# Performance work log

Measured on AMD Instinct MI355X. Metric: run time of the kernel, lower is better.

The kernel has to match this reference:

```python
import jax, jax.numpy as jnp
import numpy as np

D_MODEL = 512; D_STATE = 32; D_HEAD = 64; G = 4; R = 2
D_INNER = 2 * D_MODEL            # expand=2 -> 1024
H = D_INNER // D_HEAD            # 16 heads
RATIO = H // G                   # 4 heads per group
CHUNK = 128; EPS = 1e-5
DIM_Z = D_INNER; DIM_X = D_INNER
DIM_B = G * D_STATE * R; DIM_C = DIM_B
D_PROJ = DIM_Z + DIM_X + DIM_B + DIM_C + G + G
BATCH = 1; SEQ = 2048


def setup_inputs() -> dict:
    key = jax.random.key(0)
    ks = jax.random.split(key, 10)
    u = jax.random.normal(ks[0], (BATCH, SEQ, D_MODEL), jnp.float32)
    W_in = jax.random.normal(ks[1], (D_MODEL, D_PROJ), jnp.float32) * 0.02
    b_in = jnp.zeros((D_PROJ,), jnp.float32)
    # dt bias init: inverse-softplus of log-uniform dt in [1e-3, 1e-1]
    dt0 = jnp.exp(jax.random.uniform(ks[2], (G,)) * (np.log(0.1) - np.log(0.001)) + np.log(0.001))
    inv_dt = dt0 + jnp.log(-jnp.expm1(-dt0))
    s = DIM_Z + DIM_X + DIM_B + DIM_C
    b_in = b_in.at[s:s + G].set(inv_dt).at[s + G:].set(-3.0)
    W_xup = jax.random.normal(ks[3], (D_HEAD, D_HEAD * R), jnp.float32) * (1.0 / np.sqrt(D_HEAD * R))
    W_ydown = jax.random.normal(ks[4], (D_HEAD * R, D_HEAD), jnp.float32) * (1.0 / np.sqrt(D_HEAD * R))
    A_log = jnp.log(jax.random.uniform(ks[5], (G,), minval=1.0, maxval=16.0))
    theta_log = jax.random.normal(ks[6], (G, D_STATE // 2), jnp.float32)
    D_param = jnp.ones((H,), jnp.float32)
    wB = jnp.ones((D_STATE * R,), jnp.float32)
    wC = jnp.ones((D_STATE * R,), jnp.float32)
    bias_B = jnp.ones((G, D_STATE, R), jnp.float32)
    bias_C = jnp.ones((G, D_STATE, R), jnp.float32)
    W_out = jax.random.normal(ks[7], (D_INNER, D_MODEL), jnp.float32) * 0.02
    return dict(u=u, W_in=W_in, b_in=b_in, W_xup=W_xup, W_ydown=W_ydown,
                A_log=A_log, theta_log=theta_log, D_param=D_param,
                wB=wB, wC=wC, bias_B=bias_B, bias_C=bias_C, W_out=W_out)


def rmsnorm(x, w):
    return x * jax.lax.rsqrt(jnp.mean(x * x, -1, keepdims=True) + EPS) * w


def apply_rope(x, angles):
    # x: (B,L,G,N,R)  angles: (B,L,G,N/2)  -- rotate (even, odd) pairs along N
    Bz, L, Gg, N, Rr = x.shape
    xr = x.reshape(Bz, L, Gg, N // 2, 2, Rr)
    re, im = xr[..., 0, :], xr[..., 1, :]
    c = jnp.cos(angles)[..., None]
    s = jnp.sin(angles)[..., None]
    out = jnp.stack([re * c - im * s, re * s + im * c], axis=-2)
    return out.reshape(Bz, L, Gg, N, Rr)


def segsum(x):
    # x: (..., T) log-decay -> (..., T, T) causal pairwise cumulative sums
    T = x.shape[-1]
    cs = jnp.cumsum(x, -1)
    seg = cs[..., :, None] - cs[..., None, :]
    mask = jnp.tril(jnp.ones((T, T), bool))
    return jnp.where(mask, seg, -jnp.inf)


def chunk_parallel_scan(u_in, dt, A, C):
    # u_in: (B,L,H,N,P)  dt: (B,L,H)  A: (H,)  C: (B,L,H,N,R)
    Bz, L, Hh, N, P = u_in.shape
    Rr = C.shape[-1]
    nc = L // CHUNK
    la = (dt * A).reshape(Bz, nc, CHUNK, Hh)                       # log alpha per chunk
    uc = u_in.reshape(Bz, nc, CHUNK, Hh, N, P)
    Cc = C.reshape(Bz, nc, CHUNK, Hh, N, Rr)
    Lm = jnp.exp(segsum(la.transpose(0, 1, 3, 2)))                 # (B,nc,H,cs,cs)
    h_intra = jnp.einsum('bchts,bcshnp->bcthnp', Lm, uc)           # intra-chunk states
    y_diag = jnp.einsum('bcthnp,bcthnr->bcthpr', h_intra, Cc)
    decay_chunk = jnp.exp(la.sum(2))                               # (B,nc,H)
    h_final = h_intra[:, :, -1]                                    # (B,nc,H,N,P)
    h0 = jnp.zeros((Bz, Hh, N, P), u_in.dtype)

    def step(h, inp):
        d, c = inp
        return h * d[..., None, None] + c, h

    h_last, h_states = jax.lax.scan(
        step, h0, (decay_chunk.transpose(1, 0, 2), h_final.transpose(1, 0, 2, 3, 4)))
    h_states = h_states.transpose(1, 0, 2, 3, 4)                   # state entering each chunk
    decay_intra = jnp.exp(jnp.cumsum(la, 2))                       # (B,nc,cs,H)
    C_scaled = Cc * decay_intra[..., None, None]
    y_off = jnp.einsum('bchnp,bcthnr->bcthpr', h_states, C_scaled)
    y = (y_diag + y_off).reshape(Bz, L, Hh, P, Rr)
    return y, h_last


def _forward(u, W_in, b_in, W_xup, W_ydown, A_log, theta_log, D_param, wB, wC, bias_B, bias_C, W_out):
    Bz, L, _ = u.shape
    N, P = D_STATE, D_HEAD
    proj = u @ W_in + b_in
    o = 0
    z = proj[..., o:o + DIM_Z]; o += DIM_Z
    x = proj[..., o:o + DIM_X]; o += DIM_X
    Bi = proj[..., o:o + DIM_B]; o += DIM_B
    Ci = proj[..., o:o + DIM_C]; o += DIM_C
    dt_raw = proj[..., o:o + G]; o += G
    lam_raw = proj[..., o:o + G]

    dt = jax.nn.softplus(dt_raw)                                   # (B,L,G)
    lam = jax.nn.sigmoid(lam_raw)                                  # trapezoidal coeff
    x = jax.nn.silu(x)

    Bm = rmsnorm(Bi.reshape(Bz, L, G, N * R), wB).reshape(Bz, L, G, N, R) + bias_B
    Cm = rmsnorm(Ci.reshape(Bz, L, G, N * R), wC).reshape(Bz, L, G, N, R) + bias_C

    # data-dependent RoPE: cumulative angles = cumsum_t(dt_t * theta)
    theta = jnp.exp(theta_log)                                     # (G, N/2)
    angles = jnp.cumsum(dt[..., None] * theta, axis=1)             # (B,L,G,N/2)
    Br = apply_rope(Bm, angles)
    Cr = apply_rope(Cm, angles)

    # expand group-shared dynamics to heads
    Bh = jnp.repeat(Br, RATIO, axis=2)                             # (B,L,H,N,R)
    Ch = jnp.repeat(Cr, RATIO, axis=2)
    dth = jnp.repeat(dt, RATIO, axis=2)                            # (B,L,H)
    lamh = jnp.repeat(lam, RATIO, axis=2)
    Ah = jnp.repeat(-jnp.exp(A_log), RATIO)                        # (H,)

    xh = x.reshape(Bz, L, H, P)
    x_up = (xh @ W_xup).reshape(Bz, L, H, P, R)                    # MIMO up-projection
    u_ssm = jnp.einsum('blhnr,blhpr->blhnp', Bh, x_up) * dth[..., None, None]
    # generalized trapezoidal rule: blend current and previous input contribution
    u_prev = jnp.pad(u_ssm[:, :-1], ((0, 0), (1, 0), (0, 0), (0, 0), (0, 0)))
    w = lamh[..., None, None]
    u_trap = w * u_ssm + (1.0 - w) * u_prev

    y, _h = chunk_parallel_scan(u_trap, dth, Ah, Ch)               # (B,L,H,P,R)
    y = y.reshape(Bz, L, H, P * R) @ W_ydown                       # MIMO down-projection
    y = y + D_param[None, None, :, None] * xh                      # skip connection
    y = y * jax.nn.silu(z.reshape(Bz, L, H, P))                    # gate
    return (y.reshape(Bz, L, D_INNER)) @ W_out


def reference(u, W_in, b_in, W_xup, W_ydown, A_log, theta_log, D_param, wB, wC, bias_B, bias_C, W_out):
    return _forward(u, W_in, b_in, W_xup, W_ydown, A_log, theta_log,
                    D_param, wB, wC, bias_B, bias_C, W_out)
```

## Files before the change

### kernel.cpp

```cpp
#include <hip/hip_runtime.h>
#include <hip/hip_bf16.h>

typedef __hip_bfloat16 bf16;
typedef __bf16 bfv8 __attribute__((ext_vector_type(8)));
typedef float fv4 __attribute__((ext_vector_type(4)));

__device__ __forceinline__ float bf2f(bf16 x){ return __bfloat162float(x); }
__device__ __forceinline__ bf16 f2bf(float x){ return __float2bfloat16(x); }
__device__ __forceinline__ float blo(unsigned u){ return __uint_as_float(u<<16); }
__device__ __forceinline__ float bhi(unsigned u){ return __uint_as_float(u & 0xffff0000u); }
struct __align__(8) bf4v { bf16 x,y,z,w; };
struct __align__(16) bf8s { ushort u[8]; };
__device__ __forceinline__ float4 ldb4(const bf16* p){
  ushort4 u = *(const ushort4*)p;
  float4 r;
  r.x = __uint_as_float(((unsigned)u.x)<<16);
  r.y = __uint_as_float(((unsigned)u.y)<<16);
  r.z = __uint_as_float(((unsigned)u.z)<<16);
  r.w = __uint_as_float(((unsigned)u.w)<<16);
  return r;
}
__device__ __forceinline__ void stb4(bf16* p, float4 v){
  bf4v t; t.x=f2bf(v.x); t.y=f2bf(v.y); t.z=f2bf(v.z); t.w=f2bf(v.w);
  *(bf4v*)p = t;
}

#define L_SEQ 2048
#define DPROJ 2568
#define NCHUNK 16
#define TCH 128

__device__ __forceinline__ void tbody(const float* __restrict__ in, bf16* __restrict__ out,
                                      int R, int C, int Cpad, int bx, int by, float (*t)[33])
{
  int c0 = bx*32, r0 = by*32;
  int tx = threadIdx.x & 31, ty = threadIdx.x >> 5;
  for (int i=0;i<32;i+=8){
    int r = r0+i+ty, cc = c0+tx;
    t[i+ty][tx] = (r<R && cc<C) ? in[(size_t)r*C+cc] : 0.f;
  }
  __syncthreads();
  for (int i=0;i<32;i+=8){
    int cc = c0+i+ty, r = r0+tx;
    if (cc<Cpad && r<R) out[(size_t)cc*R + r] = f2bf(t[tx][i+ty]);
  }
}

__global__ void prep(const float* __restrict__ u, bf16* __restrict__ ubf,
                     const float* __restrict__ Win, bf16* __restrict__ WinT,
                     const float* __restrict__ Wout, bf16* __restrict__ WoutT,
                     const float* __restrict__ Wyd, bf16* __restrict__ WydT)
{
  __shared__ float t[32][33];
  int b = blockIdx.x;
  if (b < 1024){
    int i = (b*256 + threadIdx.x)*4;
    float4 v = *(const float4*)&u[i];
    stb4(&ubf[i], v);
  } else if (b < 2368){
    int idx = b - 1024;
    tbody(Win, WinT, 512, DPROJ, 2688, idx%84, idx/84, t);
  } else if (b < 2880){
    int idx = b - 2368;
    tbody(Wout, WoutT, 1024, 512, 512, idx%16, idx/16, t);
  } else {
    int idx = b - 2880;
    tbody(Wyd, WydT, 128, 64, 64, idx%2, idx/2, t);
  }
}

__global__ void __launch_bounds__(256) gemm1_mfma(const bf16* __restrict__ A, const bf16* __restrict__ BT,
                                                  const float* __restrict__ bias, bf16* __restrict__ C,
                                                  float* __restrict__ side)
{
  const int K = 512;
  __shared__ __align__(16) bf16 As[128*40];
  __shared__ __align__(16) bf16 Bs[128*40];
  int tid = threadIdx.x;
  int col0 = blockIdx.x*128, row0 = blockIdx.y*128;
  int wid = tid>>6, lane = tid&63;
  int wm = (wid&1)*64, wn = (wid>>1)*64;
  int lm = lane&15, lq = lane>>4;
  fv4 acc[4][4] = {};
  for (int k0=0;k0<K;k0+=32){
    #pragma unroll
    for (int i=0;i<2;i++){
      int e = tid + i*256;
      int r = e>>2, k8 = (e&3)*8;
      *(bf8s*)&As[r*40+k8] = *(const bf8s*)&A[(size_t)(row0+r)*K + k0 + k8];
      *(bf8s*)&Bs[r*40+k8] = *(const bf8s*)&BT[(size_t)(col0+r)*K + k0 + k8];
    }
    __syncthreads();
    bfv8 af[4], bfr[4];
    #pragma unroll
    for (int mf=0;mf<4;mf++) af[mf] = *(const bfv8*)&As[(wm+mf*16+lm)*40 + lq*8];
    #pragma unroll
    for (int nf=0;nf<4;nf++) bfr[nf] = *(const bfv8*)&Bs[(wn+nf*16+lm)*40 + lq*8];
    #pragma unroll
    for (int mf=0;mf<4;mf++)
      #pragma unroll
      for (int nf=0;nf<4;nf++)
        acc[mf][nf] = __builtin_amdgcn_mfma_f32_16x16x32_bf16(af[mf], bfr[nf], acc[mf][nf], 0,0,0);
    __syncthreads();
  }
  #pragma unroll
  for (int mf=0;mf<4;mf++){
    #pragma unroll
    for (int nf=0;nf<4;nf++){
      int gcol = col0 + wn + nf*16 + lm;
      if (gcol < DPROJ){
        float bia = bias[gcol];
        #pragma unroll
        for (int r=0;r<4;r++){
          int grow = row0 + wm + mf*16 + lq*4 + r;
          float v = acc[mf][nf][r] + bia;
          C[(size_t)grow*DPROJ + gcol] = f2bf(v);
          if (gcol >= 2560) side[grow*8 + (gcol-2560)] = v;
        }
      }
    }
  }
}

__global__ void __launch_bounds__(256) gemmo_mfma(const bf16* __restrict__ Yp, const bf16* __restrict__ BT,
                                                  float* __restrict__ C)
{
  const int K = 1024;
  __shared__ __align__(16) bf16 As[64*40];
  __shared__ __align__(16) bf16 Bs[64*40];
  int tid = threadIdx.x;
  int col0 = blockIdx.x*64, row0 = blockIdx.y*64;
  int wid = tid>>6, lane = tid&63;
  int wm = (wid&1)*32, wn = (wid>>1)*32;
  int lm = lane&15, lq = lane>>4;
  fv4 acc[2][2] = {};
  for (int k0=0;k0<K;k0+=32){
    {
      int m = tid>>2, k8 = (tid&3)*8;
      int kg = k0 + k8;
      *(bf8s*)&As[m*40+k8] = *(const bf8s*)&Yp[(size_t)(row0+m)*2048 + ((kg>>6)*128) + 64 + (kg&63)];
    }
    {
      int n = tid>>2, k8 = (tid&3)*8;
      *(bf8s*)&Bs[n*40+k8] = *(const bf8s*)&BT[(size_t)(col0+n)*K + k0 + k8];
    }
    __syncthreads();
    bfv8 af[2], bfr[2];
    #pragma unroll
    for (int mf=0;mf<2;mf++) af[mf] = *(const bfv8*)&As[(wm+mf*16+lm)*40 + lq*8];
    #pragma unroll
    for (int nf=0;nf<2;nf++) bfr[nf] = *(const bfv8*)&Bs[(wn+nf*16+lm)*40 + lq*8];
    #pragma unroll
    for (int mf=0;mf<2;mf++)
      #pragma unroll
      for (int nf=0;nf<2;nf++)
        acc[mf][nf] = __builtin_amdgcn_mfma_f32_16x16x32_bf16(af[mf], bfr[nf], acc[mf][nf], 0,0,0);
    __syncthreads();
  }
  #pragma unroll
  for (int mf=0;mf<2;mf++)
    #pragma unroll
    for (int nf=0;nf<2;nf++){
      int gcol = col0 + wn + nf*16 + lm;
      #pragma unroll
      for (int r=0;r<4;r++){
        int grow = row0 + wm + mf*16 + lq*4 + r;
        C[(size_t)grow*512 + gcol] = acc[mf][nf][r];
      }
    }
}

__global__ void k23(const float* __restrict__ dlraw, float* __restrict__ dtb,
                    float* __restrict__ lamb, float* __restrict__ csdt)
{
  __shared__ float raw[L_SEQ*8];
  __shared__ float dts[L_SEQ*4];
  __shared__ float segs[4][64];
  int tid = threadIdx.x;
  for (int e=tid;e<L_SEQ*8;e+=256) raw[e] = dlraw[e];
  __syncthreads();
  int g = tid & 3, seg = tid >> 2;
  for (int i = 0; i < 32; i++){
    int l = seg*32 + i;
    float dr = raw[l*8 + g];
    float lr = raw[l*8 + 4 + g];
    float dt = (dr > 15.f) ? dr : log1pf(__expf(dr));
    dts[l*4+g] = dt;
    dtb[l*4+g] = dt;
    lamb[l*4+g] = 1.f/(1.f+__expf(-lr));
  }
  __syncthreads();
  float s = 0.f;
  for (int i=0;i<32;i++) s += dts[(seg*32+i)*4 + g];
  segs[g][seg] = s;
  __syncthreads();
  if (tid < 4) { float run = 0.f; for (int q=0;q<64;q++){ float t = segs[tid][q]; segs[tid][q] = run; run += t; } }
  __syncthreads();
  float run = segs[g][seg];
  for (int i=0;i<32;i++){ int l = seg*32+i; run += dts[l*4+g]; csdt[l*4+g] = run; }
}

__global__ void __launch_bounds__(256) k45(
  const bf16* __restrict__ proj, const float* __restrict__ wB, const float* __restrict__ wC,
  const float* __restrict__ biasB, const float* __restrict__ biasC,
  const float* __restrict__ theta_log, const float* __restrict__ csdt,
  const float* __restrict__ Wx,
  bf16* __restrict__ Br, bf16* __restrict__ Cr, bf16* __restrict__ xup)
{
  __shared__ __align__(16) float wsm[64*128];
  __shared__ float xs[1024];
  int l = blockIdx.x, tid = threadIdx.x;
  const bf16* pr = proj + (size_t)l*DPROJ;
  for (int e=tid;e<8192;e+=256) wsm[e] = Wx[e];
  for (int e=tid;e<1024;e+=256){ float v = bf2f(pr[1024+e]); xs[e] = v/(1.f+__expf(-v)); }
  {
    int g = tid >> 6, idx = tid & 63;
    float bv = bf2f(pr[2048 + g*64 + idx]);
    float cv = bf2f(pr[2304 + g*64 + idx]);
    float sb = bv*bv, sc = cv*cv;
    #pragma unroll
    for (int off=32; off; off>>=1){ sb += __shfl_xor(sb, off); sc += __shfl_xor(sc, off); }
    float rb = rsqrtf(sb*(1.f/64.f) + 1e-5f);
    float rc = rsqrtf(sc*(1.f/64.f) + 1e-5f);
    float bm = bv*rb*wB[idx] + biasB[g*64+idx];
    float cm = cv*rc*wC[idx] + biasC[g*64+idx];
    int k = idx >> 2;
    float ang = csdt[l*4+g] * __expf(theta_log[g*16+k]);
    float ca = cosf(ang), sa = sinf(ang);
    float bp = __shfl_xor(bm, 2);
    float cp = __shfl_xor(cm, 2);
    bool is_im = (idx >> 1) & 1;
    float bo = is_im ? (bp*sa + bm*ca) : (bm*ca - bp*sa);
    float co = is_im ? (cp*sa + cm*ca) : (cm*ca - cp*sa);
    Br[((size_t)l*4+g)*64 + idx] = f2bf(bo);
    Cr[((size_t)l*4+g)*64 + idx] = f2bf(co);
  }
  __syncthreads();
  {
    int h = tid>>4, prb = (tid&15)*8;
    float acc[8] = {};
    for (int k=0;k<64;k++){
      float xv = xs[h*64+k];
      const float4* w4 = (const float4*)&wsm[k*128 + prb];
      float4 a = w4[0], b = w4[1];
      acc[0]+=xv*a.x; acc[1]+=xv*a.y; acc[2]+=xv*a.z; acc[3]+=xv*a.w;
      acc[4]+=xv*b.x; acc[5]+=xv*b.y; acc[6]+=xv*b.z; acc[7]+=xv*b.w;
    }
    bf16* o = xup + ((size_t)l*16+h)*128 + prb;
    stb4(o,   make_float4(acc[0],acc[1],acc[2],acc[3]));
    stb4(o+4, make_float4(acc[4],acc[5],acc[6],acc[7]));
  }
}

__global__ void __launch_bounds__(256) k6y(
  const bf16* __restrict__ Br, const bf16* __restrict__ Cr, const bf16* __restrict__ xup,
  const float* __restrict__ dtb, const float* __restrict__ lamb, const float* __restrict__ A_log,
  bf16* __restrict__ ypr, bf16* __restrict__ hfin, float* __restrict__ dcb, float* __restrict__ csb)
{
  __shared__ __align__(16) bf16 Cs[64*40];
  __shared__ __align__(16) bf16 Bs[64*40];
  __shared__ __align__(16) bf16 Bsn[32*72];
  __shared__ __align__(16) bf16 Fs[64*72];
  __shared__ __align__(16) bf16 Xs[64*72];
  __shared__ float dt_l[128], lam_l[128], cs_l[128];
  __shared__ float u1s[160], u12s[160], vs_[32];
  int bx = blockIdx.x; int g = bx & 3, q = bx >> 2;
  int c = blockIdx.y;
  int h4 = blockIdx.z;
  int h = g*4 + h4;
  int tid = threadIdx.x;
  int l0 = c*TCH;
  int w = tid>>6, lane = tid&63, lm = lane&15, lq = lane>>4;
  float Ah = -__expf(A_log[g]);
  float dt_prev = (c>0) ? dtb[(l0-1)*4+g] : 0.f;
  if (tid<128){ dt_l[tid] = dtb[(l0+tid)*4+g]; lam_l[tid] = lamb[(l0+tid)*4+g]; }
  __syncthreads();
  if (tid<128) cs_l[tid] = dt_l[tid]*Ah;
  __syncthreads();
  for (int off=1; off<128; off<<=1){
    float add = 0.f;
    if (tid<128 && tid>=off) add = cs_l[tid-off];
    __syncthreads();
    if (tid<128) cs_l[tid] += add;
    __syncthreads();
  }
  float ref = cs_l[q*32+16];
  if (tid < 160){
    int jj = tid;
    float u1v = 0.f, u2v = 0.f;
    if (jj>=1 && jj<=128) u1v = lam_l[jj-1]*dt_l[jj-1]*__expf(fminf(ref-cs_l[jj-1],60.f));
    if (jj<=127){ float dtx = (jj>=1)? dt_l[jj-1] : dt_prev; u2v = (1.f-lam_l[jj])*dtx*__expf(fminf(ref-cs_l[jj],60.f)); }
    u1s[jj] = u1v; u12s[jj] = u1v+u2v;
  }
  if (tid < 32) vs_[tid] = __expf(fminf(cs_l[q*32+tid]-ref,60.f));
  for (int e4 = tid; e4 < 512; e4 += 256){
    int tl = e4>>4, c4 = (e4&15)*4;
    bf4v v = *(const bf4v*)&Cr[((size_t)(l0+q*32+tl)*4+g)*64 + c4];
    bf16 arr[4] = {v.x,v.y,v.z,v.w};
    #pragma unroll
    for (int i=0;i<4;i++){ int q6=c4+i; Cs[((tl<<1)|(q6&1))*40 + (q6>>1)] = arr[i]; }
  }
  __syncthreads();
  float vfin = __expf(fminf(cs_l[127]-ref,60.f));
  fv4 acc[4] = {};
  fv4 acch[2] = {};
  int nch = (q+2 < 5) ? (q+2) : 5;
  for (int kc=0; kc<nch; kc++){
    for (int e4 = tid; e4 < 512; e4 += 256){
      int jjloc = e4>>4, c4 = (e4&15)*4;
      int jj = kc*32 + jjloc; int l = l0-1+jj;
      bf4v v;
      if (l >= 0 && jj <= 128) v = *(const bf4v*)&Br[((size_t)l*4+g)*64 + c4];
      else { v.x=v.y=v.z=v.w = f2bf(0.f); }
      bf16 arr[4] = {v.x,v.y,v.z,v.w};
      #pragma unroll
      for (int i=0;i<4;i++){ int q6=c4+i; Bs[((q6&1)*32+jjloc)*40 + (q6>>1)] = arr[i]; }
      if (q == 3){
        float gcv = vfin * u12s[jj];
        #pragma unroll
        for (int i=0;i<4;i++){ int q6=c4+i; Bsn[(q6>>1)*72 + (q6&1)*32 + jjloc] = f2bf(gcv*bf2f(arr[i])); }
      }
    }
    for (int e4 = tid; e4 < 1024; e4 += 256){
      int jjloc = e4>>5, c4 = (e4&31)*4;
      int jj = kc*32+jjloc; int l = l0-1+jj;
      bf4v v;
      if (l>=0 && jj<=128) v = *(const bf4v*)&xup[((size_t)l*16 + h)*128 + c4];
      else { v.x=v.y=v.z=v.w = f2bf(0.f); }
      bf16 arr[4] = {v.x,v.y,v.z,v.w};
      #pragma unroll
      for (int i=0;i<4;i++){ int q7=c4+i; Xs[(q7>>1)*72 + (q7&1)*32 + jjloc] = arr[i]; }
    }
    __syncthreads();
    {
      bfv8 a = *(const bfv8*)&Cs[(w*16+lm)*40 + lq*8];
      fv4 zz = {0.f,0.f,0.f,0.f};
      int rb = w*16 + lq*4;
      float vA = vs_[rb>>1];
      float vB = vs_[(rb>>1)+1];
      #pragma unroll
      for (int nt=0;nt<4;nt++){
        bfv8 b = *(const bfv8*)&Bs[(nt*16+lm)*40 + lq*8];
        fv4 s = __builtin_amdgcn_mfma_f32_16x16x32_bf16(a, b, zz, 0,0,0);
        int col = nt*16+lm;
        int jj = kc*32 + (col&31);
        float u1v = u1s[jj], u12v = u12s[jj];
        #pragma unroll
        for (int r=0;r<4;r++){
          int row = rb + r;
          float vT = (r<2) ? vA : vB;
          float cf;
          if (kc < q) cf = u12v;
          else {
            int T = q*32 + (row>>1);
            if (kc == q) cf = (jj<=T) ? u12v : ((jj==T+1) ? u1v : 0.f);
            else         cf = (jj==T+1) ? u1v : 0.f;
          }
          Fs[row*72+col] = f2bf(cf*vT*s[r]);
        }
      }
    }
    __syncthreads();
    #pragma unroll
    for (int r2=0;r2<2;r2++){
      bfv8 a = *(const bfv8*)&Fs[(w*16+lm)*72 + r2*32 + lq*8];
      #pragma unroll
      for (int nt=0;nt<4;nt++){
        bfv8 b = *(const bfv8*)&Xs[(nt*16+lm)*72 + r2*32 + lq*8];
        acc[nt] = __builtin_amdgcn_mfma_f32_16x16x32_bf16(a, b, acc[nt], 0,0,0);
      }
    }
    if (q == 3){
      #pragma unroll
      for (int r2=0;r2<2;r2++){
        bfv8 a = *(const bfv8*)&Xs[(w*16+lm)*72 + r2*32 + lq*8];
        #pragma unroll
        for (int nt2=0;nt2<2;nt2++){
          bfv8 b = *(const bfv8*)&Bsn[(nt2*16+lm)*72 + r2*32 + lq*8];
          acch[nt2] = __builtin_amdgcn_mfma_f32_16x16x32_bf16(a, b, acch[nt2], 0,0,0);
        }
      }
    }
    __syncthreads();
  }
  #pragma unroll
  for (int nt=0;nt<4;nt++){
    int p = nt*16+lm;
    #pragma unroll
    for (int r=0;r<4;r++){
      int row = w*16+lq*4+r;
      int T = q*32+(row>>1), r1 = row&1;
      ypr[((size_t)(l0+T)*16 + h)*128 + p*2+r1] = f2bf(acc[nt][r]);
    }
  }
  if (q == 3){
    #pragma unroll
    for (int nt2=0;nt2<2;nt2++){
      int n = nt2*16+lm;
      #pragma unroll
      for (int r=0;r<4;r++){
        int p = w*16+lq*4+r;
        hfin[(((size_t)c*16+h)*64 + p)*32 + n] = f2bf(acch[nt2][r]);
      }
    }
    if (tid == 0) dcb[c*16+h] = __expf(cs_l[127]);
  }
  if (q == 0 && h4 == 0 && tid < 128) csb[(c*4+g)*128 + tid] = cs_l[tid];
}

__global__ void __launch_bounds__(256) k8af(
  const bf16* __restrict__ Cr, const bf16* __restrict__ hfin,
  const float* __restrict__ dcb, const float* __restrict__ csb,
  bf16* __restrict__ ypr, const bf16* __restrict__ WydT,
  const bf16* __restrict__ proj, const float* __restrict__ Dp)
{
  __shared__ __align__(16) char arena[52224];
  bf16* C2s = (bf16*)arena;
  bf16* hT  = (bf16*)(arena + 20480);
  float* cse = (float*)(arena + 25600);
  bf16* Yf  = (bf16*)arena;
  bf16* Wds = (bf16*)(arena + 34816);
  int h = blockIdx.x, c = blockIdx.y;
  int g = h >> 2;
  int tid = threadIdx.x;
  int l0 = c*TCH;
  int w = tid>>6, lane = tid&63, lm = lane&15, lq = lane>>4;
  for (int e4 = tid; e4 < 2048; e4 += 256){
    int tl = e4>>4, c4 = (e4&15)*4;
    bf4v v = *(const bf4v*)&Cr[((size_t)(l0+tl)*4+g)*64 + c4];
    bf16 arr[4] = {v.x,v.y,v.z,v.w};
    #pragma unroll
    for (int i=0;i<4;i++){ int q6=c4+i; C2s[((tl<<1)|(q6&1))*40 + (q6>>1)] = arr[i]; }
  }
  for (int e = tid; e < 1024; e += 256){
    int qq = e>>4, k8 = (e&15)*8;
    *(bf8s*)&Wds[qq*136 + k8] = *(const bf8s*)&WydT[qq*128 + k8];
  }
  {
    int e0 = tid*8;
    float carry[8] = {};
    for (int j = 0; j < c; j++){
      float dc = dcb[j*16+h];
      float4 a = ldb4(&hfin[((size_t)j*16+h)*2048 + e0]);
      float4 b = ldb4(&hfin[((size_t)j*16+h)*2048 + e0 + 4]);
      carry[0]=carry[0]*dc+a.x; carry[1]=carry[1]*dc+a.y; carry[2]=carry[2]*dc+a.z; carry[3]=carry[3]*dc+a.w;
      carry[4]=carry[4]*dc+b.x; carry[5]=carry[5]*dc+b.y; carry[6]=carry[6]*dc+b.z; carry[7]=carry[7]*dc+b.w;
    }
    int p = e0>>5, n = e0&31;
    stb4(&hT[p*40+n],   make_float4(carry[0],carry[1],carry[2],carry[3]));
    stb4(&hT[p*40+n+4], make_float4(carry[4],carry[5],carry[6],carry[7]));
  }
  if (tid < 128) cse[tid] = __expf(csb[(c*4+g)*128 + tid]);
  __syncthreads();
  float yfull[4][4][4];
  fv4 zz = {0.f,0.f,0.f,0.f};
  #pragma unroll
  for (int mi=0;mi<4;mi++){
    int mt = w*4 + mi;
    bfv8 a = *(const bfv8*)&C2s[(mt*16+lm)*40 + lq*8];
    #pragma unroll
    for (int nt=0;nt<4;nt++){
      bfv8 b = *(const bfv8*)&hT[(nt*16+lm)*40 + lq*8];
      fv4 s = __builtin_amdgcn_mfma_f32_16x16x32_bf16(a, b, zz, 0,0,0);
      int p = nt*16+lm;
      #pragma unroll
      for (int r=0;r<4;r++){
        int row = mt*16+lq*4+r;
        int tl = row>>1, r1 = row&1;
        float yd = bf2f(ypr[((size_t)(l0+tl)*16 + h)*128 + p*2 + r1]);
        yfull[mi][nt][r] = yd + cse[tl]*s[r];
      }
    }
  }
  __syncthreads();
  #pragma unroll
  for (int mi=0;mi<4;mi++){
    int mt = w*4 + mi;
    #pragma unroll
    for (int nt=0;nt<4;nt++){
      int p = nt*16+lm;
      #pragma unroll
      for (int r=0;r<4;r++){
        int row = mt*16+lq*4+r;
        int tl = row>>1, r1 = row&1;
        Yf[tl*136 + p*2 + r1] = f2bf(yfull[mi][nt][r]);
      }
    }
  }
  __syncthreads();
  fv4 acc2[2][4] = {};
  #pragma unroll
  for (int kq=0;kq<4;kq++){
    #pragma unroll
    for (int m2=0;m2<2;m2++){
      bfv8 a = *(const bfv8*)&Yf[((w*2+m2)*16+lm)*136 + kq*32 + lq*8];
      #pragma unroll
      for (int nt2=0;nt2<4;nt2++){
        bfv8 b = *(const bfv8*)&Wds[(nt2*16+lm)*136 + kq*32 + lq*8];
        acc2[m2][nt2] = __builtin_amdgcn_mfma_f32_16x16x32_bf16(a, b, acc2[m2][nt2], 0,0,0);
      }
    }
  }
  float dv = Dp[h];
  #pragma unroll
  for (int m2=0;m2<2;m2++){
    #pragma unroll
    for (int nt2=0;nt2<4;nt2++){
      int qq = nt2*16+lm;
      #pragma unroll
      for (int r=0;r<4;r++){
        int tl = (w*2+m2)*16 + lq*4 + r;
        size_t lrow = (size_t)(l0+tl)*DPROJ;
        float x = bf2f(proj[lrow + 1024 + h*64 + qq]);
        float z = bf2f(proj[lrow + h*64 + qq]);
        float xs = x/(1.f+__expf(-x));
        float zs = z/(1.f+__expf(-z));
        float outv = (acc2[m2][nt2][r] + dv*xs)*zs;
        ypr[((size_t)(l0+tl)*16 + h)*128 + 64 + qq] = f2bf(outv);
      }
    }
  }
}

extern "C" void kernel_launch(void* const* d_in, const int* in_sizes, int n_in,
                              void* d_out, int out_size, void* d_ws, size_t ws_size,
                              hipStream_t stream) {
  const float* u       = (const float*)d_in[0];
  const float* W_in    = (const float*)d_in[1];
  const float* b_in    = (const float*)d_in[2];
  const float* W_xup   = (const float*)d_in[3];
  const float* W_ydown = (const float*)d_in[4];
  const float* A_log   = (const float*)d_in[5];
  const float* theta_l = (const float*)d_in[6];
  const float* D_p     = (const float*)d_in[7];
  const float* wB      = (const float*)d_in[8];
  const float* wC      = (const float*)d_in[9];
  const float* biasB   = (const float*)d_in[10];
  const float* biasC   = (const float*)d_in[11];
  const float* W_out   = (const float*)d_in[12];
  float* out = (float*)d_out;

  char* w = (char*)d_ws;
  bf16*  proj  = (bf16*)(w);
  float* dlraw = (float*)(w + 10518528);
  float* dtb   = (float*)(w + 10584064);
  float* lamb  = (float*)(w + 10616832);
  float* csdt  = (float*)(w + 10649600);
  bf16*  Brb   = (bf16*)(w + 10682368);
  bf16*  Crb   = (bf16*)(w + 11730944);
  bf16*  xupb  = (bf16*)(w + 12779520);
  bf16*  hfin  = (bf16*)(w + 21168128);
  float* dcb   = (float*)(w + 23265280);
  float* csb   = (float*)(w + 23266304);
  bf16*  ypr   = (bf16*)(w + 23299072);
  bf16*  WinT  = (bf16*)(w + 23299072);
  bf16*  ubf   = (bf16*)(w + 31687680);
  bf16*  WoutT = (bf16*)(w + 33784832);
  bf16*  WydT  = (bf16*)(w + 34833408);

  prep<<<2888,256,0,stream>>>(u, ubf, W_in, WinT, W_out, WoutT, W_ydown, WydT);
  gemm1_mfma<<<dim3(21,16),256,0,stream>>>(ubf, WinT, b_in, proj, dlraw);
  k23<<<1,256,0,stream>>>(dlraw, dtb, lamb, csdt);
  k45<<<2048,256,0,stream>>>(proj, wB, wC, biasB, biasC, theta_l, csdt, W_xup, Brb, Crb, xupb);
  k6y<<<dim3(16,16,4),256,0,stream>>>(Brb, Crb, xupb, dtb, lamb, A_log, ypr, hfin, dcb, csb);
  k8af<<<dim3(16,16),256,0,stream>>>(Crb, hfin, dcb, csb, ypr, WydT, proj, D_p);
  gemmo_mfma<<<dim3(8,32),256,0,stream>>>(ypr, WoutT, out);
}
```

Baseline: 205.0 us.

## Precompute chunk decay scan in separate kernel and widen output GEMM K-tile

Moves the per-chunk cumulative decay scan and the trapezoid weight, decay-vector and final-decay computation out of k6y into a new small kernel k23b. Previously every one of 1024 k6y blocks redid a 128-element log-step scan with many barriers. k6y now just loads the precomputed tables, and k8af reads a per-group decay instead of a per-head one. Separately, the output GEMM now stages 64-wide K tiles, halving the number of barrier pairs per K loop. The cost is an extra kernel launch and small global buffers.

```diff
diff --git a/kernel.cpp b/kernel.cpp
--- a/kernel.cpp
+++ b/kernel.cpp
@@ -126,35 +126,37 @@
                                                   float* __restrict__ C)
 {
   const int K = 1024;
-  __shared__ __align__(16) bf16 As[64*40];
-  __shared__ __align__(16) bf16 Bs[64*40];
+  __shared__ __align__(16) bf16 As[64*72];
+  __shared__ __align__(16) bf16 Bs[64*72];
   int tid = threadIdx.x;
   int col0 = blockIdx.x*64, row0 = blockIdx.y*64;
   int wid = tid>>6, lane = tid&63;
   int wm = (wid&1)*32, wn = (wid>>1)*32;
   int lm = lane&15, lq = lane>>4;
   fv4 acc[2][2] = {};
-  for (int k0=0;k0<K;k0+=32){
-    {
-      int m = tid>>2, k8 = (tid&3)*8;
+  for (int k0=0;k0<K;k0+=64){
+    #pragma unroll
+    for (int i=0;i<2;i++){
+      int e = tid + i*256;
+      int m = e>>3, k8 = (e&7)*8;
       int kg = k0 + k8;
-      *(bf8s*)&As[m*40+k8] = *(const bf8s*)&Yp[(size_t)(row0+m)*2048 + ((kg>>6)*128) + 64 + (kg&63)];
-    }
-    {
-      int n = tid>>2, k8 = (tid&3)*8;
-      *(bf8s*)&Bs[n*40+k8] = *(const bf8s*)&BT[(size_t)(col0+n)*K + k0 + k8];
-    }
-    __syncthreads();
-    bfv8 af[2], bfr[2];
-    #pragma unroll
-    for (int mf=0;mf<2;mf++) af[mf] = *(const bfv8*)&As[(wm+mf*16+lm)*40 + lq*8];
-    #pragma unroll
-    for (int nf=0;nf<2;nf++) bfr[nf] = *(const bfv8*)&Bs[(wn+nf*16+lm)*40 + lq*8];
-    #pragma unroll
-    for (int mf=0;mf<2;mf++)
-      #pragma unroll
-      for (int nf=0;nf<2;nf++)
-        acc[mf][nf] = __builtin_amdgcn_mfma_f32_16x16x32_bf16(af[mf], bfr[nf], acc[mf][nf], 0,0,0);
+      *(bf8s*)&As[m*72+k8] = *(const bf8s*)&Yp[(size_t)(row0+m)*2048 + ((kg>>6)*128) + 64 + (kg&63)];
+      *(bf8s*)&Bs[m*72+k8] = *(const bf8s*)&BT[(size_t)(col0+m)*K + kg];
+    }
+    __syncthreads();
+    #pragma unroll
+    for (int kq=0;kq<2;kq++){
+      bfv8 af[2], bfr[2];
+      #pragma unroll
+      for (int mf=0;mf<2;mf++) af[mf] = *(const bfv8*)&As[(wm+mf*16+lm)*72 + kq*32 + lq*8];
+      #pragma unroll
+      for (int nf=0;nf<2;nf++) bfr[nf] = *(const bfv8*)&Bs[(wn+nf*16+lm)*72 + kq*32 + lq*8];
+      #pragma unroll
+      for (int mf=0;mf<2;mf++)
+        #pragma unroll
+        for (int nf=0;nf<2;nf++)
+          acc[mf][nf] = __builtin_amdgcn_mfma_f32_16x16x32_bf16(af[mf], bfr[nf], acc[mf][nf], 0,0,0);
+    }
     __syncthreads();
   }
   #pragma unroll
@@ -198,6 +200,49 @@
   __syncthreads();
   float run = segs[g][seg];
   for (int i=0;i<32;i++){ int l = seg*32+i; run += dts[l*4+g]; csdt[l*4+g] = run; }
+}
+
+__global__ void k23b(const float* __restrict__ dtb, const float* __restrict__ lamb,
+                     const float* __restrict__ A_log,
+                     float* __restrict__ u1b, float* __restrict__ u12b,
+                     float* __restrict__ vsb, float* __restrict__ vfinb,
+                     float* __restrict__ dcg, float* __restrict__ csb)
+{
+  __shared__ float dt_l[129], lam_l[129], cs_l[128];
+  int c = blockIdx.x, g = blockIdx.y;
+  int tid = threadIdx.x;
+  int l0 = c*TCH;
+  float Ah = -__expf(A_log[g]);
+  if (tid < 129){
+    int l = l0 - 1 + tid;
+    dt_l[tid]  = (l>=0) ? dtb[l*4+g]  : 0.f;
+    lam_l[tid] = (l>=0) ? lamb[l*4+g] : 0.f;
+  }
+  __syncthreads();
+  if (tid < 128) cs_l[tid] = dt_l[tid+1]*Ah;
+  __syncthreads();
+  for (int off=1; off<128; off<<=1){
+    float add = 0.f;
+    if (tid<128 && tid>=off) add = cs_l[tid-off];
+    __syncthreads();
+    if (tid<128) cs_l[tid] += add;
+    __syncthreads();
+  }
+  if (tid == 0) dcg[c*4+g] = __expf(cs_l[127]);
+  if (tid < 128) csb[(c*4+g)*128 + tid] = cs_l[tid];
+  __syncthreads();
+  int q = tid>>6, ln = tid&63;
+  int base = ((c*4+g)*4+q)*160;
+  float ref = cs_l[q*32+16];
+  for (int jj = ln; jj < 160; jj += 64){
+    float u1v = 0.f, u2v = 0.f;
+    if (jj>=1 && jj<=128) u1v = lam_l[jj]*dt_l[jj]*__expf(fminf(ref-cs_l[jj-1],60.f));
+    if (jj<=127) u2v = (1.f-lam_l[jj+1])*dt_l[jj]*__expf(fminf(ref-cs_l[jj],60.f));
+    u1b[base+jj] = u1v;
+    u12b[base+jj] = u1v + u2v;
+  }
+  if (ln < 32) vsb[((c*4+g)*4+q)*32 + ln] = __expf(fminf(cs_l[q*32+ln]-ref,60.f));
+  if (ln == 0) vfinb[(c*4+g)*4+q] = __expf(fminf(cs_l[127]-ref,60.f));
 }
 
 __global__ void __launch_bounds__(256) k45(
@@ -254,15 +299,15 @@
 
 __global__ void __launch_bounds__(256) k6y(
   const bf16* __restrict__ Br, const bf16* __restrict__ Cr, const bf16* __restrict__ xup,
-  const float* __restrict__ dtb, const float* __restrict__ lamb, const float* __restrict__ A_log,
-  bf16* __restrict__ ypr, bf16* __restrict__ hfin, float* __restrict__ dcb, float* __restrict__ csb)
+  const float* __restrict__ u1b, const float* __restrict__ u12b,
+  const float* __restrict__ vsb, const float* __restrict__ vfinb,
+  bf16* __restrict__ ypr, bf16* __restrict__ hfin)
 {
   __shared__ __align__(16) bf16 Cs[64*40];
   __shared__ __align__(16) bf16 Bs[64*40];
   __shared__ __align__(16) bf16 Bsn[32*72];
   __shared__ __align__(16) bf16 Fs[64*72];
   __shared__ __align__(16) bf16 Xs[64*72];
-  __shared__ float dt_l[128], lam_l[128], cs_l[128];
   __shared__ float u1s[160], u12s[160], vs_[32];
   int bx = blockIdx.x; int g = bx & 3, q = bx >> 2;
   int c = blockIdx.y;
@@ -271,28 +316,10 @@
   int tid = threadIdx.x;
   int l0 = c*TCH;
   int w = tid>>6, lane = tid&63, lm = lane&15, lq = lane>>4;
-  float Ah = -__expf(A_log[g]);
-  float dt_prev = (c>0) ? dtb[(l0-1)*4+g] : 0.f;
-  if (tid<128){ dt_l[tid] = dtb[(l0+tid)*4+g]; lam_l[tid] = lamb[(l0+tid)*4+g]; }
-  __syncthreads();
-  if (tid<128) cs_l[tid] = dt_l[tid]*Ah;
-  __syncthreads();
-  for (int off=1; off<128; off<<=1){
-    float add = 0.f;
-    if (tid<128 && tid>=off) add = cs_l[tid-off];
-    __syncthreads();
-    if (tid<128) cs_l[tid] += add;
-    __syncthreads();
-  }
-  float ref = cs_l[q*32+16];
-  if (tid < 160){
-    int jj = tid;
-    float u1v = 0.f, u2v = 0.f;
-    if (jj>=1 && jj<=128) u1v = lam_l[jj-1]*dt_l[jj-1]*__expf(fminf(ref-cs_l[jj-1],60.f));
-    if (jj<=127){ float dtx = (jj>=1)? dt_l[jj-1] : dt_prev; u2v = (1.f-lam_l[jj])*dtx*__expf(fminf(ref-cs_l[jj],60.f)); }
-    u1s[jj] = u1v; u12s[jj] = u1v+u2v;
-  }
-  if (tid < 32) vs_[tid] = __expf(fminf(cs_l[q*32+tid]-ref,60.f));
+  int idx = ((c*4+g)*4+q);
+  if (tid < 160){ u1s[tid] = u1b[idx*160+tid]; u12s[tid] = u12b[idx*160+tid]; }
+  if (tid < 32) vs_[tid] = vsb[idx*32+tid];
+  float vfin = vfinb[idx];
   for (int e4 = tid; e4 < 512; e4 += 256){
     int tl = e4>>4, c4 = (e4&15)*4;
     bf4v v = *(const bf4v*)&Cr[((size_t)(l0+q*32+tl)*4+g)*64 + c4];
@@ -301,7 +328,6 @@
     for (int i=0;i<4;i++){ int q6=c4+i; Cs[((tl<<1)|(q6&1))*40 + (q6>>1)] = arr[i]; }
   }
   __syncthreads();
-  float vfin = __expf(fminf(cs_l[127]-ref,60.f));
   fv4 acc[4] = {};
   fv4 acch[2] = {};
   int nch = (q+2 < 5) ? (q+2) : 5;
@@ -403,14 +429,12 @@
         hfin[(((size_t)c*16+h)*64 + p)*32 + n] = f2bf(acch[nt2][r]);
       }
     }
-    if (tid == 0) dcb[c*16+h] = __expf(cs_l[127]);
-  }
-  if (q == 0 && h4 == 0 && tid < 128) csb[(c*4+g)*128 + tid] = cs_l[tid];
+  }
 }
 
 __global__ void __launch_bounds__(256) k8af(
   const bf16* __restrict__ Cr, const bf16* __restrict__ hfin,
-  const float* __restrict__ dcb, const float* __restrict__ csb,
+  const float* __restrict__ dcg, const float* __restrict__ csb,
   bf16* __restrict__ ypr, const bf16* __restrict__ WydT,
   const bf16* __restrict__ proj, const float* __restrict__ Dp)
 {
@@ -440,7 +464,7 @@
     int e0 = tid*8;
     float carry[8] = {};
     for (int j = 0; j < c; j++){
-      float dc = dcb[j*16+h];
+      float dc = dcg[j*4+g];
       float4 a = ldb4(&hfin[((size_t)j*16+h)*2048 + e0]);
       float4 b = ldb4(&hfin[((size_t)j*16+h)*2048 + e0 + 4]);
       carry[0]=carry[0]*dc+a.x; carry[1]=carry[1]*dc+a.y; carry[2]=carry[2]*dc+a.z; carry[3]=carry[3]*dc+a.w;
@@ -550,19 +574,24 @@
   bf16*  Crb   = (bf16*)(w + 11730944);
   bf16*  xupb  = (bf16*)(w + 12779520);
   bf16*  hfin  = (bf16*)(w + 21168128);
-  float* dcb   = (float*)(w + 23265280);
   float* csb   = (float*)(w + 23266304);
   bf16*  ypr   = (bf16*)(w + 23299072);
   bf16*  WinT  = (bf16*)(w + 23299072);
   bf16*  ubf   = (bf16*)(w + 31687680);
   bf16*  WoutT = (bf16*)(w + 33784832);
   bf16*  WydT  = (bf16*)(w + 34833408);
+  float* u1b   = (float*)(w + 34849792);
+  float* u12b  = (float*)(w + 35013632);
+  float* vsb   = (float*)(w + 35177472);
+  float* vfinb = (float*)(w + 35210240);
+  float* dcg   = (float*)(w + 35211264);
 
   prep<<<2888,256,0,stream>>>(u, ubf, W_in, WinT, W_out, WoutT, W_ydown, WydT);
   gemm1_mfma<<<dim3(21,16),256,0,stream>>>(ubf, WinT, b_in, proj, dlraw);
   k23<<<1,256,0,stream>>>(dlraw, dtb, lamb, csdt);
+  k23b<<<dim3(16,4),256,0,stream>>>(dtb, lamb, A_log, u1b, u12b, vsb, vfinb, dcg, csb);
   k45<<<2048,256,0,stream>>>(proj, wB, wC, biasB, biasC, theta_l, csdt, W_xup, Brb, Crb, xupb);
-  k6y<<<dim3(16,16,4),256,0,stream>>>(Brb, Crb, xupb, dtb, lamb, A_log, ypr, hfin, dcb, csb);
-  k8af<<<dim3(16,16),256,0,stream>>>(Crb, hfin, dcb, csb, ypr, WydT, proj, D_p);
+  k6y<<<dim3(16,16,4),256,0,stream>>>(Brb, Crb, xupb, u1b, u12b, vsb, vfinb, ypr, hfin);
+  k8af<<<dim3(16,16),256,0,stream>>>(Crb, hfin, dcg, csb, ypr, WydT, proj, D_p);
   gemmo_mfma<<<dim3(8,32),256,0,stream>>>(ypr, WoutT, out);
 }
```

New measurement: 217.8 us. 1.06x slower.
